# Kernel tuning notes

Hardware: AMD Instinct MI355X
Metric: run time of the kernel (lower is better)

The kernel has to match this reference:

```python
import jax, jax.numpy as jnp
import numpy as np
import math

N = 64
DIN = 2
DOUT = 2
D = 4
BATCH = 16384
EPS_DIV = 1e-6


def setup_inputs() -> dict:
    key = jax.random.key(0)
    k1, k2, k3 = jax.random.split(key, 3)
    x = jax.random.normal(k1, (BATCH, N, DIN), jnp.float32)
    # A scaled by 0.5 to keep 64-step products of DxD matrices inside float32 range
    A = jax.random.normal(k2, (N, D, D, DIN), jnp.float32) * 0.5
    B = jax.random.normal(k3, (N, D, D, DOUT, DIN), jnp.float32)
    scale = jnp.ones((1,), jnp.float32)
    return {"x": x, "A": A, "B": B, "scale": scale}


def _forward(x, A, B, scale):
    b, n, din = x.shape
    nbin = int(math.log(n - 1) / math.log(2.0)) + 1  # matches torch set_parallel_vars
    s = scale.reshape(())
    # per-site L2 normalization of input features (torch: X / ||X||, no eps)
    xn = x / jnp.linalg.norm(x, axis=-1, keepdims=True)
    M = jnp.einsum('bni,nlri->nblr', xn, A)  # [n, b, D, D] site matrices
    # binary tree of pairwise products: levels[l] has (n >> l) blocks covering 2^l sites
    levels = [M]
    cur = M
    for _ in range(nbin - 1):
        m = cur.shape[0]
        pair = cur.reshape(m // 2, 2, b, D, D)
        cur = jnp.einsum('pbij,pbjk->pbik', pair[:, 0], pair[:, 1])
        levels.append(cur)
    idx = jnp.arange(n)
    # Left prefix boundary vectors: vL[i] = e0^T * prod_{k<i} M_k (i=0 unused).
    # Built by walking the set bits of i (MSB->LSB), exactly like the torch
    # Bleft[nbin-1-j][xp[j]] indexing, but vectorized over all i at once.
    vL = jnp.zeros((n, b, D), M.dtype)
    startedL = jnp.zeros((n,), bool)
    for j in range(nbin):
        l = nbin - 1 - j                 # tree level for bit j
        bit = ((idx >> l) & 1).astype(bool)
        blk = 2 * (idx >> (l + 1))       # == xp[j] in torch
        Bl = levels[l][blk]              # [n, b, D, D]
        init = Bl[:, :, 0, :]            # left boundary row e0^T A
        step = jnp.einsum('nbi,nbij->nbj', vL, Bl)
        new = jnp.where(startedL[:, None, None], step, init)
        vL = jnp.where(bit[:, None, None], new, vL)
        startedL = startedL | bit
    vL = vL / (jnp.linalg.norm(vL, axis=-1, keepdims=True) + EPS_DIV)
    # Right suffix boundary vectors: vR[i] = (prod_{k=n-i}^{n-1} M_k) e0 (i=0 unused).
    # For n a power of two, Bright levels coincide with Bleft levels.
    vR = jnp.zeros((n, b, D), M.dtype)
    startedR = jnp.zeros((n,), bool)
    for j in range(nbin):
        l = nbin - 1 - j
        bit = ((idx >> l) & 1).astype(bool)
        nblk = n >> l
        blk = nblk - 1 - 2 * (idx >> (l + 1))  # index from the right end
        Bl = levels[l][blk]
        init = Bl[:, :, :, 0]            # right boundary column A e0
        step = jnp.einsum('nbij,nbj->nbi', Bl, vR)
        new = jnp.where(startedR[:, None, None], step, init)
        vR = jnp.where(bit[:, None, None], new, vR)
        startedR = startedR | bit
    vR = vR / (jnp.linalg.norm(vR, axis=-1, keepdims=True) + EPS_DIV)
    Aright = vR[::-1]  # Aright[i] = vR[n-1-i], valid for sites 0..n-2
    # Local operators H_i: boundary-contracted MPO tensors
    Hmid = jnp.einsum('nbi,niljk,nbl->nbjk', vL[1:n - 1], B[1:n - 1], Aright[1:n - 1])
    H0 = jnp.einsum('ljk,bl->bjk', B[0, 0], Aright[0])
    Hlast = jnp.einsum('bi,ijk->bjk', vL[n - 1], B[n - 1, :, 0])
    H = jnp.concatenate([H0[None], Hmid, Hlast[None]], axis=0)  # [n, b, dout, din]
    nrm = jnp.sqrt(jnp.sum(H * H, axis=(-2, -1), keepdims=True)) + EPS_DIV
    H = s * (H / nrm)
    H = jnp.where(jnp.isnan(H), 0.0, H)
    H = jax.nn.relu(H)                   # activation='relu'
    # apply local operator to normalized local input; out_norm='none'
    y = jnp.einsum('nbjk,bnk->bnj', H, xn)  # [b, n, dout]
    return y


def reference(x, A, B, scale):
    return _forward(x, A, B, scale)
```

## Files before the change

### kernel.cpp

```cpp
#include <hip/hip_runtime.h>
#include <math.h>


#define EPS 1e-6f
#define RSQ(x) __builtin_amdgcn_rsqf((x) + 1e-30f)

__global__ __launch_bounds__(512, 2)
void tdvp_kernel(const float* __restrict__ x,
                 const float* __restrict__ A,
                 const float* __restrict__ Bw,
                 const float* __restrict__ scale,
                 float* __restrict__ y)
{
    __shared__ float sU[8320];

    const int tid = threadIdx.x;
    const int bb  = tid & 63;
    const int s   = __builtin_amdgcn_readfirstlane(tid >> 6);

    {
        const float4* xg = (const float4*)x + (size_t)blockIdx.x * 2048;
        #pragma unroll
        for (int it = 0; it < 4; ++it) {
            const int g = it * 512 + tid;
            const float4 v = xg[g];
            const int c = g >> 5, f = (g & 31) * 4;
            *(float2*)&sU[c * 130 + f]     = make_float2(v.x, v.y);
            *(float2*)&sU[c * 130 + f + 2] = make_float2(v.z, v.w);
        }
    }
    __syncthreads();

    const int n0 = s * 8;
    float xa[8], xc[8];
    #pragma unroll
    for (int k = 0; k < 8; ++k) {
        const float2 v = *(const float2*)&sU[bb * 130 + n0 * 2 + 2 * k];
        const float inr = RSQ(v.x * v.x + v.y * v.y);
        xa[k] = v.x * inr; xc[k] = v.y * inr;
    }
    __syncthreads();

    float M[8][16];
    #pragma unroll
    for (int k = 0; k < 8; ++k) {
        const float* Ak = A + (size_t)(n0 + k) * 32;
        #pragma unroll
        for (int e = 0; e < 16; ++e)
            M[k][e] = fmaf(xc[k], Ak[2 * e + 1], xa[k] * Ak[2 * e]);
    }

    {
        float P[16];
        #pragma unroll
        for (int e = 0; e < 16; ++e) P[e] = M[0][e];
        #pragma unroll
        for (int k = 1; k < 8; ++k) {
            float Pn[16];
            #pragma unroll
            for (int i = 0; i < 4; ++i) {
                #pragma unroll
                for (int j = 0; j < 4; ++j) {
                    float acc = P[i*4] * M[k][j];
                    acc = fmaf(P[i*4+1], M[k][4+j],  acc);
                    acc = fmaf(P[i*4+2], M[k][8+j],  acc);
                    acc = fmaf(P[i*4+3], M[k][12+j], acc);
                    Pn[i*4+j] = acc;
                }
            }
            #pragma unroll
            for (int e = 0; e < 16; ++e) P[e] = Pn[e];
        }
        float ss = 0.f;
        #pragma unroll
        for (int e = 0; e < 16; ++e) ss = fmaf(P[e], P[e], ss);
        const float rn = RSQ(ss);
        #pragma unroll
        for (int e = 0; e < 16; ++e)
            sU[s * 1024 + e * 64 + bb] = P[e] * rn;
    }
    __syncthreads();

    float v0 = 1.f, v1 = 0.f, v2 = 0.f, v3 = 0.f;
    #pragma unroll 1
    for (int t = 0; t < s; ++t) {
        const float* pp = &sU[t * 1024 + bb];
        const float p0  = pp[0],      p1  = pp[64],     p2  = pp[128],    p3  = pp[192];
        const float p4  = pp[256],    p5  = pp[320],    p6  = pp[384],    p7  = pp[448];
        const float p8  = pp[512],    p9  = pp[576],    p10 = pp[640],    p11 = pp[704];
        const float p12 = pp[768],    p13 = pp[832],    p14 = pp[896],    p15 = pp[960];
        const float w0 = v0*p0 + v1*p4 + v2*p8  + v3*p12;
        const float w1 = v0*p1 + v1*p5 + v2*p9  + v3*p13;
        const float w2 = v0*p2 + v1*p6 + v2*p10 + v3*p14;
        const float w3 = v0*p3 + v1*p7 + v2*p11 + v3*p15;
        const float rn = RSQ(w0*w0 + w1*w1 + w2*w2 + w3*w3);
        v0 = w0*rn; v1 = w1*rn; v2 = w2*rn; v3 = w3*rn;
    }
    float u0 = 1.f, u1 = 0.f, u2 = 0.f, u3 = 0.f;
    #pragma unroll 1
    for (int t = 7; t > s; --t) {
        const float* pp = &sU[t * 1024 + bb];
        const float p0  = pp[0],      p1  = pp[64],     p2  = pp[128],    p3  = pp[192];
        const float p4  = pp[256],    p5  = pp[320],    p6  = pp[384],    p7  = pp[448];
        const float p8  = pp[512],    p9  = pp[576],    p10 = pp[640],    p11 = pp[704];
        const float p12 = pp[768],    p13 = pp[832],    p14 = pp[896],    p15 = pp[960];
        const float w0 = p0*u0  + p1*u1  + p2*u2  + p3*u3;
        const float w1 = p4*u0  + p5*u1  + p6*u2  + p7*u3;
        const float w2 = p8*u0  + p9*u1  + p10*u2 + p11*u3;
        const float w3 = p12*u0 + p13*u1 + p14*u2 + p15*u3;
        const float rn = RSQ(w0*w0 + w1*w1 + w2*w2 + w3*w3);
        u0 = w0*rn; u1 = w1*rn; u2 = w2*rn; u3 = w3*rn;
    }

    float vlA[8], vlB[8], vlC[8], vlD[8];
    {
        float a0 = v0, a1 = v1, a2 = v2, a3 = v3;
        #pragma unroll
        for (int k = 0; k < 8; ++k) {
            vlA[k] = a0; vlB[k] = a1; vlC[k] = a2; vlD[k] = a3;
            if (k == 7) break;
            const float t0 = a0*M[k][0] + a1*M[k][4] + a2*M[k][8]  + a3*M[k][12];
            const float t1 = a0*M[k][1] + a1*M[k][5] + a2*M[k][9]  + a3*M[k][13];
            const float t2 = a0*M[k][2] + a1*M[k][6] + a2*M[k][10] + a3*M[k][14];
            const float t3 = a0*M[k][3] + a1*M[k][7] + a2*M[k][11] + a3*M[k][15];
            a0 = t0; a1 = t1; a2 = t2; a3 = t3;
        }
    }
    __syncthreads();

    const float sc = scale[0];
    #pragma unroll
    for (int kk = 7; kk >= 0; --kk) {
        const int n = n0 + kk;

        const float arn = RSQ(u0*u0 + u1*u1 + u2*u2 + u3*u3);
        float aa0 = u0*arn, aa1 = u1*arn, aa2 = u2*arn, aa3 = u3*arn;
        if (n == 63) { aa0 = 1.f; aa1 = aa2 = aa3 = 0.f; }

        const float wn = RSQ(vlA[kk]*vlA[kk] + vlB[kk]*vlB[kk] +
                             vlC[kk]*vlC[kk] + vlD[kk]*vlD[kk]);
        float vv0 = vlA[kk]*wn, vv1 = vlB[kk]*wn, vv2 = vlC[kk]*wn, vv3 = vlD[kk]*wn;
        if (n == 0) { vv0 = 1.f; vv1 = vv2 = vv3 = 0.f; }

        const float vv[4] = {vv0, vv1, vv2, vv3};
        const float aa[4] = {aa0, aa1, aa2, aa3};
        const float* Bn = Bw + (size_t)n * 64;
        float H00 = 0.f, H01 = 0.f, H10 = 0.f, H11 = 0.f;
        #pragma unroll
        for (int i = 0; i < 4; ++i) {
            #pragma unroll
            for (int l = 0; l < 4; ++l) {
                const float c = vv[i] * aa[l];
                const int   q = (i * 4 + l) * 4;
                H00 = fmaf(c, Bn[q + 0], H00);
                H01 = fmaf(c, Bn[q + 1], H01);
                H10 = fmaf(c, Bn[q + 2], H10);
                H11 = fmaf(c, Bn[q + 3], H11);
            }
        }
        const float rh = sc * RSQ(H00*H00 + H01*H01 + H10*H10 + H11*H11);
        H00 *= rh; H01 *= rh; H10 *= rh; H11 *= rh;
        if (__builtin_isnan(H00)) H00 = 0.f;
        if (__builtin_isnan(H01)) H01 = 0.f;
        if (__builtin_isnan(H10)) H10 = 0.f;
        if (__builtin_isnan(H11)) H11 = 0.f;
        H00 = fmaxf(H00, 0.f); H01 = fmaxf(H01, 0.f);
        H10 = fmaxf(H10, 0.f); H11 = fmaxf(H11, 0.f);

        float2 yo;
        yo.x = fmaf(H01, xc[kk], H00 * xa[kk]);
        yo.y = fmaf(H11, xc[kk], H10 * xa[kk]);
        *(float2*)&sU[bb * 130 + 2 * n] = yo;

        if (kk > 0) {
            const float t0 = M[kk][0]*u0  + M[kk][1]*u1  + M[kk][2]*u2  + M[kk][3]*u3;
            const float t1 = M[kk][4]*u0  + M[kk][5]*u1  + M[kk][6]*u2  + M[kk][7]*u3;
            const float t2 = M[kk][8]*u0  + M[kk][9]*u1  + M[kk][10]*u2 + M[kk][11]*u3;
            const float t3 = M[kk][12]*u0 + M[kk][13]*u1 + M[kk][14]*u2 + M[kk][15]*u3;
            u0 = t0; u1 = t1; u2 = t2; u3 = t3;
        }
    }
    __syncthreads();

    {
        float4* yg = (float4*)y + (size_t)blockIdx.x * 2048;
        #pragma unroll
        for (int it = 0; it < 4; ++it) {
            const int g = it * 512 + tid;
            const int c = g >> 5, f = (g & 31) * 4;
            const float2 a = *(const float2*)&sU[c * 130 + f];
            const float2 b = *(const float2*)&sU[c * 130 + f + 2];
            yg[g] = make_float4(a.x, a.y, b.x, b.y);
        }
    }
}

extern "C" void kernel_launch(void* const* d_in, const int* in_sizes, int n_in,
                              void* d_out, int out_size, void* d_ws, size_t ws_size,
                              hipStream_t stream) {
    const float* x     = (const float*)d_in[0];
    const float* A     = (const float*)d_in[1];
    const float* B     = (const float*)d_in[2];
    const float* scale = (const float*)d_in[3];
    float* yp = (float*)d_out;
    const int batch  = in_sizes[0] / 128;
    const int blocks = batch / 64;
    tdvp_kernel<<<blocks, 512, 0, stream>>>(x, A, B, scale, yp);
}
```

Baseline: 77.75 us.

## Split sites across 16 waves and recompute site matrices to cut registers

Block size goes from 512 to 1024 threads, so each wave now handles 4 sites instead of 8. The per-site 4x4 matrices are rebuilt from A and the normalized inputs wherever they are needed instead of being held in a large register array. The shared-memory layout for segment products changes to float2 interleaved reads. This is meant to lower register pressure and raise occupancy and parallelism, at the cost of recomputing the matrices and running longer sequential prefix/suffix loops over 16 segments.

```diff
diff --git a/kernel.cpp b/kernel.cpp
--- a/kernel.cpp
+++ b/kernel.cpp
@@ -5,14 +5,21 @@
 #define EPS 1e-6f
 #define RSQ(x) __builtin_amdgcn_rsqf((x) + 1e-30f)
 
-__global__ __launch_bounds__(512, 2)
+#define BUILD_M(Mk, Ak, xav, xcv)                                   \
+    {                                                               \
+        _Pragma("unroll")                                           \
+        for (int e = 0; e < 16; ++e)                                \
+            Mk[e] = fmaf((xcv), (Ak)[2*e+1], (xav) * (Ak)[2*e]);    \
+    }
+
+__global__ __launch_bounds__(1024, 4)
 void tdvp_kernel(const float* __restrict__ x,
                  const float* __restrict__ A,
                  const float* __restrict__ Bw,
                  const float* __restrict__ scale,
                  float* __restrict__ y)
 {
-    __shared__ float sU[8320];
+    __shared__ float sU[16384];
 
     const int tid = threadIdx.x;
     const int bb  = tid & 63;
@@ -21,8 +28,8 @@
     {
         const float4* xg = (const float4*)x + (size_t)blockIdx.x * 2048;
         #pragma unroll
-        for (int it = 0; it < 4; ++it) {
-            const int g = it * 512 + tid;
+        for (int it = 0; it < 2; ++it) {
+            const int g = it * 1024 + tid;
             const float4 v = xg[g];
             const int c = g >> 5, f = (g & 31) * 4;
             *(float2*)&sU[c * 130 + f]     = make_float2(v.x, v.y);
@@ -31,40 +38,36 @@
     }
     __syncthreads();
 
-    const int n0 = s * 8;
-    float xa[8], xc[8];
+    const int n0 = s * 4;
+    float xa[4], xc[4];
     #pragma unroll
-    for (int k = 0; k < 8; ++k) {
+    for (int k = 0; k < 4; ++k) {
         const float2 v = *(const float2*)&sU[bb * 130 + n0 * 2 + 2 * k];
         const float inr = RSQ(v.x * v.x + v.y * v.y);
         xa[k] = v.x * inr; xc[k] = v.y * inr;
     }
     __syncthreads();
 
-    float M[8][16];
-    #pragma unroll
-    for (int k = 0; k < 8; ++k) {
-        const float* Ak = A + (size_t)(n0 + k) * 32;
-        #pragma unroll
-        for (int e = 0; e < 16; ++e)
-            M[k][e] = fmaf(xc[k], Ak[2 * e + 1], xa[k] * Ak[2 * e]);
-    }
-
     {
         float P[16];
-        #pragma unroll
-        for (int e = 0; e < 16; ++e) P[e] = M[0][e];
-        #pragma unroll
-        for (int k = 1; k < 8; ++k) {
+        {
+            const float* Ak = A + (size_t)n0 * 32;
+            BUILD_M(P, Ak, xa[0], xc[0]);
+        }
+        #pragma unroll
+        for (int k = 1; k < 4; ++k) {
+            float Mk[16];
+            const float* Ak = A + (size_t)(n0 + k) * 32;
+            BUILD_M(Mk, Ak, xa[k], xc[k]);
             float Pn[16];
             #pragma unroll
             for (int i = 0; i < 4; ++i) {
                 #pragma unroll
                 for (int j = 0; j < 4; ++j) {
-                    float acc = P[i*4] * M[k][j];
-                    acc = fmaf(P[i*4+1], M[k][4+j],  acc);
-                    acc = fmaf(P[i*4+2], M[k][8+j],  acc);
-                    acc = fmaf(P[i*4+3], M[k][12+j], acc);
+                    float acc = P[i*4] * Mk[j];
+                    acc = fmaf(P[i*4+1], Mk[4+j],  acc);
+                    acc = fmaf(P[i*4+2], Mk[8+j],  acc);
+                    acc = fmaf(P[i*4+3], Mk[12+j], acc);
                     Pn[i*4+j] = acc;
                 }
             }
@@ -76,53 +79,61 @@
         for (int e = 0; e < 16; ++e) ss = fmaf(P[e], P[e], ss);
         const float rn = RSQ(ss);
         #pragma unroll
-        for (int e = 0; e < 16; ++e)
-            sU[s * 1024 + e * 64 + bb] = P[e] * rn;
+        for (int ep = 0; ep < 8; ++ep)
+            *(float2*)&sU[s * 1024 + ep * 128 + bb * 2] =
+                make_float2(P[2*ep] * rn, P[2*ep+1] * rn);
     }
     __syncthreads();
 
     float v0 = 1.f, v1 = 0.f, v2 = 0.f, v3 = 0.f;
     #pragma unroll 1
     for (int t = 0; t < s; ++t) {
-        const float* pp = &sU[t * 1024 + bb];
-        const float p0  = pp[0],      p1  = pp[64],     p2  = pp[128],    p3  = pp[192];
-        const float p4  = pp[256],    p5  = pp[320],    p6  = pp[384],    p7  = pp[448];
-        const float p8  = pp[512],    p9  = pp[576],    p10 = pp[640],    p11 = pp[704];
-        const float p12 = pp[768],    p13 = pp[832],    p14 = pp[896],    p15 = pp[960];
-        const float w0 = v0*p0 + v1*p4 + v2*p8  + v3*p12;
-        const float w1 = v0*p1 + v1*p5 + v2*p9  + v3*p13;
-        const float w2 = v0*p2 + v1*p6 + v2*p10 + v3*p14;
-        const float w3 = v0*p3 + v1*p7 + v2*p11 + v3*p15;
+        const float* pp = &sU[t * 1024 + bb * 2];
+        float p[16];
+        #pragma unroll
+        for (int ep = 0; ep < 8; ++ep) {
+            const float2 q = *(const float2*)&pp[ep * 128];
+            p[2*ep] = q.x; p[2*ep+1] = q.y;
+        }
+        const float w0 = v0*p[0] + v1*p[4] + v2*p[8]  + v3*p[12];
+        const float w1 = v0*p[1] + v1*p[5] + v2*p[9]  + v3*p[13];
+        const float w2 = v0*p[2] + v1*p[6] + v2*p[10] + v3*p[14];
+        const float w3 = v0*p[3] + v1*p[7] + v2*p[11] + v3*p[15];
         const float rn = RSQ(w0*w0 + w1*w1 + w2*w2 + w3*w3);
         v0 = w0*rn; v1 = w1*rn; v2 = w2*rn; v3 = w3*rn;
     }
     float u0 = 1.f, u1 = 0.f, u2 = 0.f, u3 = 0.f;
     #pragma unroll 1
-    for (int t = 7; t > s; --t) {
-        const float* pp = &sU[t * 1024 + bb];
-        const float p0  = pp[0],      p1  = pp[64],     p2  = pp[128],    p3  = pp[192];
-        const float p4  = pp[256],    p5  = pp[320],    p6  = pp[384],    p7  = pp[448];
-        const float p8  = pp[512],    p9  = pp[576],    p10 = pp[640],    p11 = pp[704];
-        const float p12 = pp[768],    p13 = pp[832],    p14 = pp[896],    p15 = pp[960];
-        const float w0 = p0*u0  + p1*u1  + p2*u2  + p3*u3;
-        const float w1 = p4*u0  + p5*u1  + p6*u2  + p7*u3;
-        const float w2 = p8*u0  + p9*u1  + p10*u2 + p11*u3;
-        const float w3 = p12*u0 + p13*u1 + p14*u2 + p15*u3;
+    for (int t = 15; t > s; --t) {
+        const float* pp = &sU[t * 1024 + bb * 2];
+        float p[16];
+        #pragma unroll
+        for (int ep = 0; ep < 8; ++ep) {
+            const float2 q = *(const float2*)&pp[ep * 128];
+            p[2*ep] = q.x; p[2*ep+1] = q.y;
+        }
+        const float w0 = p[0]*u0  + p[1]*u1  + p[2]*u2  + p[3]*u3;
+        const float w1 = p[4]*u0  + p[5]*u1  + p[6]*u2  + p[7]*u3;
+        const float w2 = p[8]*u0  + p[9]*u1  + p[10]*u2 + p[11]*u3;
+        const float w3 = p[12]*u0 + p[13]*u1 + p[14]*u2 + p[15]*u3;
         const float rn = RSQ(w0*w0 + w1*w1 + w2*w2 + w3*w3);
         u0 = w0*rn; u1 = w1*rn; u2 = w2*rn; u3 = w3*rn;
     }
 
-    float vlA[8], vlB[8], vlC[8], vlD[8];
+    float vlA[4], vlB[4], vlC[4], vlD[4];
     {
         float a0 = v0, a1 = v1, a2 = v2, a3 = v3;
         #pragma unroll
-        for (int k = 0; k < 8; ++k) {
+        for (int k = 0; k < 4; ++k) {
             vlA[k] = a0; vlB[k] = a1; vlC[k] = a2; vlD[k] = a3;
-            if (k == 7) break;
-            const float t0 = a0*M[k][0] + a1*M[k][4] + a2*M[k][8]  + a3*M[k][12];
-            const float t1 = a0*M[k][1] + a1*M[k][5] + a2*M[k][9]  + a3*M[k][13];
-            const float t2 = a0*M[k][2] + a1*M[k][6] + a2*M[k][10] + a3*M[k][14];
-            const float t3 = a0*M[k][3] + a1*M[k][7] + a2*M[k][11] + a3*M[k][15];
+            if (k == 3) break;
+            float Mk[16];
+            const float* Ak = A + (size_t)(n0 + k) * 32;
+            BUILD_M(Mk, Ak, xa[k], xc[k]);
+            const float t0 = a0*Mk[0] + a1*Mk[4] + a2*Mk[8]  + a3*Mk[12];
+            const float t1 = a0*Mk[1] + a1*Mk[5] + a2*Mk[9]  + a3*Mk[13];
+            const float t2 = a0*Mk[2] + a1*Mk[6] + a2*Mk[10] + a3*Mk[14];
+            const float t3 = a0*Mk[3] + a1*Mk[7] + a2*Mk[11] + a3*Mk[15];
             a0 = t0; a1 = t1; a2 = t2; a3 = t3;
         }
     }
@@ -130,7 +141,7 @@
 
     const float sc = scale[0];
     #pragma unroll
-    for (int kk = 7; kk >= 0; --kk) {
+    for (int kk = 3; kk >= 0; --kk) {
         const int n = n0 + kk;
 
         const float arn = RSQ(u0*u0 + u1*u1 + u2*u2 + u3*u3);
@@ -173,10 +184,13 @@
         *(float2*)&sU[bb * 130 + 2 * n] = yo;
 
         if (kk > 0) {
-            const float t0 = M[kk][0]*u0  + M[kk][1]*u1  + M[kk][2]*u2  + M[kk][3]*u3;
-            const float t1 = M[kk][4]*u0  + M[kk][5]*u1  + M[kk][6]*u2  + M[kk][7]*u3;
-            const float t2 = M[kk][8]*u0  + M[kk][9]*u1  + M[kk][10]*u2 + M[kk][11]*u3;
-            const float t3 = M[kk][12]*u0 + M[kk][13]*u1 + M[kk][14]*u2 + M[kk][15]*u3;
+            float Mk[16];
+            const float* Ak = A + (size_t)(n0 + kk) * 32;
+            BUILD_M(Mk, Ak, xa[kk], xc[kk]);
+            const float t0 = Mk[0]*u0  + Mk[1]*u1  + Mk[2]*u2  + Mk[3]*u3;
+            const float t1 = Mk[4]*u0  + Mk[5]*u1  + Mk[6]*u2  + Mk[7]*u3;
+            const float t2 = Mk[8]*u0  + Mk[9]*u1  + Mk[10]*u2 + Mk[11]*u3;
+            const float t3 = Mk[12]*u0 + Mk[13]*u1 + Mk[14]*u2 + Mk[15]*u3;
             u0 = t0; u1 = t1; u2 = t2; u3 = t3;
         }
     }
@@ -185,8 +199,8 @@
     {
         float4* yg = (float4*)y + (size_t)blockIdx.x * 2048;
         #pragma unroll
-        for (int it = 0; it < 4; ++it) {
-            const int g = it * 512 + tid;
+        for (int it = 0; it < 2; ++it) {
+            const int g = it * 1024 + tid;
             const int c = g >> 5, f = (g & 31) * 4;
             const float2 a = *(const float2*)&sU[c * 130 + f];
             const float2 b = *(const float2*)&sU[c * 130 + f + 2];
@@ -205,5 +219,5 @@
     float* yp = (float*)d_out;
     const int batch  = in_sizes[0] / 128;
     const int blocks = batch / 64;
-    tdvp_kernel<<<blocks, 512, 0, stream>>>(x, A, B, scale, yp);
+    tdvp_kernel<<<blocks, 1024, 0, stream>>>(x, A, B, scale, yp);
 }
```

Result: no change. 77.70 us (-0.1%).

## Split sites across 16 wavefronts per block and merge prefix/suffix scans

Applied to the files above, without the earlier changes.

Each block now uses 1024 threads (16 wavefronts), so each wavefront handles 4 sites instead of 8. This halves per-thread register state and the serial chain length inside each segment. Segment products are stored as float4 rows so the scans can read them with vector LDS loads. The separate prefix and suffix loops are fused into one 15-step loop without per-step renormalisation, which risks float range issues over longer products and diverges across wavefronts via the uniform branches.

```diff
diff --git a/kernel.cpp b/kernel.cpp
--- a/kernel.cpp
+++ b/kernel.cpp
@@ -2,17 +2,16 @@
 #include <math.h>
 
 
-#define EPS 1e-6f
 #define RSQ(x) __builtin_amdgcn_rsqf((x) + 1e-30f)
 
-__global__ __launch_bounds__(512, 2)
+__global__ __launch_bounds__(1024, 4)
 void tdvp_kernel(const float* __restrict__ x,
                  const float* __restrict__ A,
                  const float* __restrict__ Bw,
                  const float* __restrict__ scale,
                  float* __restrict__ y)
 {
-    __shared__ float sU[8320];
+    __shared__ float sU[16384];
 
     const int tid = threadIdx.x;
     const int bb  = tid & 63;
@@ -21,8 +20,8 @@
     {
         const float4* xg = (const float4*)x + (size_t)blockIdx.x * 2048;
         #pragma unroll
-        for (int it = 0; it < 4; ++it) {
-            const int g = it * 512 + tid;
+        for (int it = 0; it < 2; ++it) {
+            const int g = it * 1024 + tid;
             const float4 v = xg[g];
             const int c = g >> 5, f = (g & 31) * 4;
             *(float2*)&sU[c * 130 + f]     = make_float2(v.x, v.y);
@@ -31,23 +30,23 @@
     }
     __syncthreads();
 
-    const int n0 = s * 8;
-    float xa[8], xc[8];
+    const int n0 = s * 4;
+    float xa[4], xc[4];
     #pragma unroll
-    for (int k = 0; k < 8; ++k) {
+    for (int k = 0; k < 4; ++k) {
         const float2 v = *(const float2*)&sU[bb * 130 + n0 * 2 + 2 * k];
         const float inr = RSQ(v.x * v.x + v.y * v.y);
         xa[k] = v.x * inr; xc[k] = v.y * inr;
     }
     __syncthreads();
 
-    float M[8][16];
+    float M[4][16];
     #pragma unroll
-    for (int k = 0; k < 8; ++k) {
+    for (int k = 0; k < 4; ++k) {
         const float* Ak = A + (size_t)(n0 + k) * 32;
         #pragma unroll
         for (int e = 0; e < 16; ++e)
-            M[k][e] = fmaf(xc[k], Ak[2 * e + 1], xa[k] * Ak[2 * e]);
+            M[k][e] = fmaf(xc[k], Ak[2*e+1], xa[k] * Ak[2*e]);
     }
 
     {
@@ -55,7 +54,7 @@
         #pragma unroll
         for (int e = 0; e < 16; ++e) P[e] = M[0][e];
         #pragma unroll
-        for (int k = 1; k < 8; ++k) {
+        for (int k = 1; k < 4; ++k) {
             float Pn[16];
             #pragma unroll
             for (int i = 0; i < 4; ++i) {
@@ -76,49 +75,44 @@
         for (int e = 0; e < 16; ++e) ss = fmaf(P[e], P[e], ss);
         const float rn = RSQ(ss);
         #pragma unroll
-        for (int e = 0; e < 16; ++e)
-            sU[s * 1024 + e * 64 + bb] = P[e] * rn;
+        for (int q = 0; q < 4; ++q)
+            *(float4*)&sU[s * 1024 + q * 256 + bb * 4] =
+                make_float4(P[4*q]*rn, P[4*q+1]*rn, P[4*q+2]*rn, P[4*q+3]*rn);
     }
     __syncthreads();
 
     float v0 = 1.f, v1 = 0.f, v2 = 0.f, v3 = 0.f;
+    float u0 = 1.f, u1 = 0.f, u2 = 0.f, u3 = 0.f;
+    const int nsuf = 15 - s;
     #pragma unroll 1
-    for (int t = 0; t < s; ++t) {
-        const float* pp = &sU[t * 1024 + bb];
-        const float p0  = pp[0],      p1  = pp[64],     p2  = pp[128],    p3  = pp[192];
-        const float p4  = pp[256],    p5  = pp[320],    p6  = pp[384],    p7  = pp[448];
-        const float p8  = pp[512],    p9  = pp[576],    p10 = pp[640],    p11 = pp[704];
-        const float p12 = pp[768],    p13 = pp[832],    p14 = pp[896],    p15 = pp[960];
-        const float w0 = v0*p0 + v1*p4 + v2*p8  + v3*p12;
-        const float w1 = v0*p1 + v1*p5 + v2*p9  + v3*p13;
-        const float w2 = v0*p2 + v1*p6 + v2*p10 + v3*p14;
-        const float w3 = v0*p3 + v1*p7 + v2*p11 + v3*p15;
-        const float rn = RSQ(w0*w0 + w1*w1 + w2*w2 + w3*w3);
-        v0 = w0*rn; v1 = w1*rn; v2 = w2*rn; v3 = w3*rn;
-    }
-    float u0 = 1.f, u1 = 0.f, u2 = 0.f, u3 = 0.f;
-    #pragma unroll 1
-    for (int t = 7; t > s; --t) {
-        const float* pp = &sU[t * 1024 + bb];
-        const float p0  = pp[0],      p1  = pp[64],     p2  = pp[128],    p3  = pp[192];
-        const float p4  = pp[256],    p5  = pp[320],    p6  = pp[384],    p7  = pp[448];
-        const float p8  = pp[512],    p9  = pp[576],    p10 = pp[640],    p11 = pp[704];
-        const float p12 = pp[768],    p13 = pp[832],    p14 = pp[896],    p15 = pp[960];
-        const float w0 = p0*u0  + p1*u1  + p2*u2  + p3*u3;
-        const float w1 = p4*u0  + p5*u1  + p6*u2  + p7*u3;
-        const float w2 = p8*u0  + p9*u1  + p10*u2 + p11*u3;
-        const float w3 = p12*u0 + p13*u1 + p14*u2 + p15*u3;
-        const float rn = RSQ(w0*w0 + w1*w1 + w2*w2 + w3*w3);
-        u0 = w0*rn; u1 = w1*rn; u2 = w2*rn; u3 = w3*rn;
-    }
-
-    float vlA[8], vlB[8], vlC[8], vlD[8];
+    for (int i = 0; i < 15; ++i) {
+        if (i < s) {
+            const float4* pp = (const float4*)&sU[i * 1024 + bb * 4];
+            const float4 r0 = pp[0], r1 = pp[64], r2 = pp[128], r3 = pp[192];
+            const float w0 = v0*r0.x + v1*r1.x + v2*r2.x + v3*r3.x;
+            const float w1 = v0*r0.y + v1*r1.y + v2*r2.y + v3*r3.y;
+            const float w2 = v0*r0.z + v1*r1.z + v2*r2.z + v3*r3.z;
+            const float w3 = v0*r0.w + v1*r1.w + v2*r2.w + v3*r3.w;
+            v0 = w0; v1 = w1; v2 = w2; v3 = w3;
+        }
+        if (i < nsuf) {
+            const float4* pp = (const float4*)&sU[(15 - i) * 1024 + bb * 4];
+            const float4 r0 = pp[0], r1 = pp[64], r2 = pp[128], r3 = pp[192];
+            const float w0 = r0.x*u0 + r0.y*u1 + r0.z*u2 + r0.w*u3;
+            const float w1 = r1.x*u0 + r1.y*u1 + r1.z*u2 + r1.w*u3;
+            const float w2 = r2.x*u0 + r2.y*u1 + r2.z*u2 + r2.w*u3;
+            const float w3 = r3.x*u0 + r3.y*u1 + r3.z*u2 + r3.w*u3;
+            u0 = w0; u1 = w1; u2 = w2; u3 = w3;
+        }
+    }
+
+    float vlA[4], vlB[4], vlC[4], vlD[4];
     {
         float a0 = v0, a1 = v1, a2 = v2, a3 = v3;
         #pragma unroll
-        for (int k = 0; k < 8; ++k) {
+        for (int k = 0; k < 4; ++k) {
             vlA[k] = a0; vlB[k] = a1; vlC[k] = a2; vlD[k] = a3;
-            if (k == 7) break;
+            if (k == 3) break;
             const float t0 = a0*M[k][0] + a1*M[k][4] + a2*M[k][8]  + a3*M[k][12];
             const float t1 = a0*M[k][1] + a1*M[k][5] + a2*M[k][9]  + a3*M[k][13];
             const float t2 = a0*M[k][2] + a1*M[k][6] + a2*M[k][10] + a3*M[k][14];
@@ -130,7 +124,7 @@
 
     const float sc = scale[0];
     #pragma unroll
-    for (int kk = 7; kk >= 0; --kk) {
+    for (int kk = 3; kk >= 0; --kk) {
         const int n = n0 + kk;
 
         const float arn = RSQ(u0*u0 + u1*u1 + u2*u2 + u3*u3);
@@ -185,8 +179,8 @@
     {
         float4* yg = (float4*)y + (size_t)blockIdx.x * 2048;
         #pragma unroll
-        for (int it = 0; it < 4; ++it) {
-            const int g = it * 512 + tid;
+        for (int it = 0; it < 2; ++it) {
+            const int g = it * 1024 + tid;
             const int c = g >> 5, f = (g & 31) * 4;
             const float2 a = *(const float2*)&sU[c * 130 + f];
             const float2 b = *(const float2*)&sU[c * 130 + f + 2];
@@ -205,5 +199,5 @@
     float* yp = (float*)d_out;
     const int batch  = in_sizes[0] / 128;
     const int blocks = batch / 64;
-    tdvp_kernel<<<blocks, 512, 0, stream>>>(x, A, B, scale, yp);
+    tdvp_kernel<<<blocks, 1024, 0, stream>>>(x, A, B, scale, yp);
 }
```

Measured after the change: 75.75 us. -2.6%, faster.
